# Kernel optimization log

Hardware: AMD Instinct MI355X
Metric: run time of the kernel (lower is better)

The kernel has to match this reference:

```python
import jax, jax.numpy as jnp
import numpy as np

N_EMB = 1024
N_HEADS = 16
HS = N_EMB // N_HEADS  # 64
BASE = 10000.0


def _rope_cache(T):
    # theta uses dim = n_emb (as in the source), sliced to hs//2 frequencies
    i = jnp.arange(HS // 2, dtype=jnp.float32)
    theta = BASE ** (-2.0 * i / N_EMB)            # [hs/2]
    pos = jnp.arange(T, dtype=jnp.float32)        # [T]
    ang = pos[:, None] * theta[None, :]           # [T, hs/2]
    return jnp.cos(ang), jnp.sin(ang)


def _apply_rope(x, cos, sin):
    # x: [B, T, nh, hs]; rotate consecutive pairs along hs
    b, t, nh, hs = x.shape
    xr = x.reshape(b, t, nh, hs // 2, 2)
    c = cos[None, :, None, :]
    s = sin[None, :, None, :]
    r0 = xr[..., 0] * c - xr[..., 1] * s
    r1 = xr[..., 1] * c + xr[..., 0] * s
    return jnp.stack([r0, r1], axis=-1).reshape(b, t, nh, hs)


def setup_inputs() -> dict:
    key = jax.random.key(0)
    k1, k2, k3, k4 = jax.random.split(key, 4)
    B, T = 2, 2048
    w_std = 0.02
    x = jax.random.normal(k1, (B, T, N_EMB), jnp.float32)
    Wq = jax.random.normal(k2, (N_EMB, N_EMB), jnp.float32) * w_std
    Wk = jax.random.normal(k3, (N_EMB, N_EMB), jnp.float32) * w_std
    Wv = jax.random.normal(k4, (N_EMB, N_EMB), jnp.float32) * w_std
    return {"x": x, "Wq": Wq, "Wk": Wk, "Wv": Wv}


def reference(x, Wq, Wk, Wv):
    B, T, C = x.shape
    # nn.Linear(bias=False): y = x @ W.T
    q = (x @ Wq.T).reshape(B, T, N_HEADS, HS)
    k = (x @ Wk.T).reshape(B, T, N_HEADS, HS)
    v = (x @ Wv.T).reshape(B, T, N_HEADS, HS)
    cos, sin = _rope_cache(T)
    q = _apply_rope(q, cos, sin)
    k = _apply_rope(k, cos, sin)
    # scale uses C (n_emb), as in the source (not head_size)
    wei = jnp.einsum('bqhd,bkhd->bhqk', q, k) * (C ** -0.5)  # [B, nh, T, T]
    mask = jnp.tril(jnp.ones((T, T), dtype=bool))
    wei = jnp.where(mask[None, None], wei, -jnp.inf)
    wei = jax.nn.softmax(wei, axis=-1)
    # dropout is identity in eval mode
    out = jnp.einsum('bhqk,bkhd->bqhd', wei, v).reshape(B, T, C)
    return out
```

## Files before the change

kernel.cpp:

```cpp
#include <hip/hip_runtime.h>
#include <stdint.h>

typedef unsigned short u16;
typedef __bf16 bf16x8 __attribute__((ext_vector_type(8)));
typedef unsigned short u16x8 __attribute__((ext_vector_type(8)));
typedef unsigned short u16x4 __attribute__((ext_vector_type(4)));
typedef float f32x4 __attribute__((ext_vector_type(4)));
typedef uint32_t u32v4 __attribute__((ext_vector_type(4)));

#define LOG2E 1.4426950408889634f

typedef const __attribute__((address_space(1))) uint32_t as1_u32;
typedef __attribute__((address_space(3))) uint32_t as3_u32;

__device__ __forceinline__ u16 f2bf(float f) {
  union { float f; uint32_t i; } v; v.f = f;
  uint32_t r = (v.i + 0x7fffu + ((v.i >> 16) & 1u)) >> 16;
  return (u16)r;
}
__device__ __forceinline__ float bf2f(u16 u) {
  union { uint32_t i; float f; } v; v.i = ((uint32_t)u) << 16; return v.f;
}

__device__ __forceinline__ void gld_lds16(const void* g, void* l) {
  as1_u32* gp = (as1_u32*)((uintptr_t)g);
  as3_u32* lp = (as3_u32*)(uint32_t)(uintptr_t)(l);
  __builtin_amdgcn_global_load_lds(gp, lp, 16, 0, 0);
}

__global__ __launch_bounds__(256) void f32_to_bf16(
    const float* __restrict__ x, const float* __restrict__ wq,
    const float* __restrict__ wk, const float* __restrict__ wv,
    u16* __restrict__ xc, u16* __restrict__ wqc,
    u16* __restrict__ wkc, u16* __restrict__ wvc) {
  const int z = blockIdx.y;
  const float* src = z == 0 ? x : (z == 1 ? wq : (z == 2 ? wk : wv));
  u16* dst = z == 0 ? xc : (z == 1 ? wqc : (z == 2 ? wkc : wvc));
  const int n = z == 0 ? (1 << 22) : (1 << 20);

  const int idx = (blockIdx.x * 256 + (int)threadIdx.x) * 8;
  if (idx >= n) return;
  const f32x4 a = *(const f32x4*)&src[idx];
  const f32x4 b = *(const f32x4*)&src[idx + 4];
  u16x8 o;
#pragma unroll
  for (int j = 0; j < 4; j++) { o[j] = f2bf(a[j]); o[j + 4] = f2bf(b[j]); }
  *(u16x8*)&dst[idx] = o;
}

__global__ __launch_bounds__(256) void qkv_gemm(
    const u16* __restrict__ xc, const u16* __restrict__ wqc,
    const u16* __restrict__ wkc, const u16* __restrict__ wvc,
    u16* __restrict__ qo, u16* __restrict__ ko, u16* __restrict__ vt) {
  __shared__ __align__(16) u16 As[128 * 32];
  __shared__ __align__(16) u16 Bs[128 * 32];

  const int tid = threadIdx.x;
  const int lane = tid & 63;
  const int w = tid >> 6;
  const int wm = w >> 1, wn = w & 1;
  const int quad = lane >> 4, m16 = lane & 15;
  const int which = blockIdx.z;

  const u16* __restrict__ Ap;
  const u16* __restrict__ Bp;
  int m0, n0;
  if (which == 2) {
    Ap = wvc; Bp = xc;
    m0 = blockIdx.x * 128;
    n0 = blockIdx.y * 128;
  } else {
    Ap = xc; Bp = which == 0 ? wqc : wkc;
    m0 = blockIdx.y * 128;
    n0 = blockIdx.x * 128;
  }

  const f32x4 z4 = {0.f, 0.f, 0.f, 0.f};
  f32x4 acc[4][4];
#pragma unroll
  for (int i = 0; i < 4; i++)
#pragma unroll
    for (int j = 0; j < 4; j++) acc[i][j] = z4;

  const int rowA = m0 + w * 32 + (lane >> 2);
  const int rowB = n0 + w * 32 + (lane >> 2);
  const int cch = (lane & 3) * 8;

  for (int k0 = 0; k0 < 1024; k0 += 32) {
    __syncthreads();
#pragma unroll
    for (int i = 0; i < 2; i++) {
      gld_lds16(&Ap[(size_t)(rowA + i * 16) * 1024 + k0 + cch],
                &As[(w * 32 + i * 16) * 32]);
      gld_lds16(&Bp[(size_t)(rowB + i * 16) * 1024 + k0 + cch],
                &Bs[(w * 32 + i * 16) * 32]);
    }
    __syncthreads();

    bf16x8 af[4], bfr[4];
#pragma unroll
    for (int t = 0; t < 4; t++) {
      af[t]  = *(const bf16x8*)&As[(wm * 64 + t * 16 + m16) * 32 + quad * 8];
      bfr[t] = *(const bf16x8*)&Bs[(wn * 64 + t * 16 + m16) * 32 + quad * 8];
    }
#pragma unroll
    for (int mt = 0; mt < 4; mt++)
#pragma unroll
      for (int nt = 0; nt < 4; nt++)
        acc[mt][nt] = __builtin_amdgcn_mfma_f32_16x16x32_bf16(
            af[mt], bfr[nt], acc[mt][nt], 0, 0, 0);
  }

  if (which < 2) {
    u16* __restrict__ out = which == 0 ? qo : ko;
#pragma unroll
    for (int mt = 0; mt < 4; mt++) {
      const int row = m0 + wm * 64 + mt * 16 + quad * 4;
#pragma unroll
      for (int nt = 0; nt < 4; nt++) {
        const int n = n0 + wn * 64 + nt * 16 + m16;
        f32x4 a = acc[mt][nt];
#pragma unroll
        for (int r = 0; r < 4; r++)
          out[(size_t)(row + r) * 1024 + n] = f2bf(a[r]);
      }
    }
  } else {
#pragma unroll
    for (int mt = 0; mt < 4; mt++) {
      const int row = m0 + wm * 64 + mt * 16 + quad * 4;
#pragma unroll
      for (int nt = 0; nt < 4; nt++) {
        const int n = n0 + wn * 64 + nt * 16 + m16;
        f32x4 a = acc[mt][nt];
#pragma unroll
        for (int r = 0; r < 4; r++)
          vt[(size_t)(row + r) * 4096 + n] = f2bf(a[r]);
      }
    }
  }
}

__global__ __launch_bounds__(256) void rope_inplace(u16* __restrict__ qb,
                                                    u16* __restrict__ kb) {
  u16* buf = blockIdx.y == 0 ? qb : kb;
  const int p = blockIdx.x * 256 + (int)threadIdx.x;
  const int nidx = p * 2;
  const int row = nidx >> 10;
  const int col = nidx & 1023;
  const int i = (col & 63) >> 1;
  const int t = row & 2047;
  const float theta = exp2f(-(float)i * 0.02595256324130752f);
  const float ang = (float)t * theta;
  float s, c;
  sincosf(ang, &s, &c);
  const float a0 = bf2f(buf[(size_t)row * 1024 + col]);
  const float a1 = bf2f(buf[(size_t)row * 1024 + col + 1]);
  buf[(size_t)row * 1024 + col]     = f2bf(a0 * c - a1 * s);
  buf[(size_t)row * 1024 + col + 1] = f2bf(a1 * c + a0 * s);
}

__global__ __launch_bounds__(256, 4) void flash_attn(
    const u16* __restrict__ qg, const u16* __restrict__ kg,
    const u16* __restrict__ vt, float* __restrict__ out) {
  __shared__ __align__(16) u16 Ks[128 * 72];
  __shared__ __align__(16) u16 Vs[64 * 136];

  const int tid = threadIdx.x, lane = tid & 63, w = tid >> 6;
  const int quad = lane >> 4, m16 = lane & 15;

  const int id  = (int)blockIdx.x;
  const int wid = (id & 7) * 128 + (id >> 3);
  const int uu  = wid & 31;
  const int v   = wid >> 5;
  const int qt  = (v & 1) ? (31 - uu) : uu;
  const int h   = v & 15;
  const int b   = v >> 4;

  const size_t base = (size_t)b * 2048 * 1024 + (size_t)h * 64;
  const size_t vbase = (size_t)(h * 64) * 4096 + (size_t)b * 2048;
  const float SC = 0.03125f * LOG2E;

  const f32x4 z4 = {0.f, 0.f, 0.f, 0.f};
  const int srow = tid >> 2, sc = (tid & 3) * 16;

  union { u16x8 u; bf16x8 f; } ones;
#pragma unroll
  for (int j = 0; j < 8; j++) ones.u[j] = 0x3F80;

  const int q0 = qt * 64;
  const int nr = (qt + 2) >> 1;

  const u16* qsrc = &qg[base + (size_t)(q0 + w * 16 + m16) * 1024 + quad * 8];
  const bf16x8 qf0 = *(const bf16x8*)qsrc;
  const bf16x8 qf1 = *(const bf16x8*)(qsrc + 32);

  u16x8 kr0, kr1, kr2, kr3, vr0, vr1, vr2, vr3;
  {
    const u16* ks = &kg[base + (size_t)srow * 1024 + sc];
    kr0 = *(const u16x8*)ks; kr1 = *(const u16x8*)(ks + 8);
    const u16* ks2 = ks + (size_t)64 * 1024;
    kr2 = *(const u16x8*)ks2; kr3 = *(const u16x8*)(ks2 + 8);
    const u16* vs = &vt[vbase + (size_t)srow * 4096 + sc];
    vr0 = *(const u16x8*)vs; vr1 = *(const u16x8*)(vs + 8);
    vr2 = *(const u16x8*)(vs + 64); vr3 = *(const u16x8*)(vs + 72);
  }

  f32x4 l4 = z4;
  f32x4 O[4];
#pragma unroll
  for (int d = 0; d < 4; d++) O[d] = z4;

  const int qrow0 = q0 + w * 16 + quad * 4;
  const int qcol  = q0 + w * 16 + m16;

  for (int rr = 0; rr < nr; ++rr) {
    const int k0 = rr * 128;
    if (rr) __syncthreads();
    *(u16x8*)&Ks[srow * 72 + sc] = kr0;
    *(u16x8*)&Ks[srow * 72 + sc + 8] = kr1;
    *(u16x8*)&Ks[(64 + srow) * 72 + sc] = kr2;
    *(u16x8*)&Ks[(64 + srow) * 72 + sc + 8] = kr3;
    {
      const u16x4* v0 = (const u16x4*)&vr0;
      const u16x4* v1 = (const u16x4*)&vr1;
      *(u16x4*)&Vs[srow * 136 + sc]      = v0[0];
      *(u16x4*)&Vs[srow * 136 + sc + 4]  = v1[0];
      *(u16x4*)&Vs[srow * 136 + sc + 8]  = v0[1];
      *(u16x4*)&Vs[srow * 136 + sc + 12] = v1[1];
      const u16x4* v2 = (const u16x4*)&vr2;
      const u16x4* v3 = (const u16x4*)&vr3;
      *(u16x4*)&Vs[srow * 136 + 64 + sc]      = v2[0];
      *(u16x4*)&Vs[srow * 136 + 64 + sc + 4]  = v3[0];
      *(u16x4*)&Vs[srow * 136 + 64 + sc + 8]  = v2[1];
      *(u16x4*)&Vs[srow * 136 + 64 + sc + 12] = v3[1];
    }
    __syncthreads();
    if (rr + 1 < nr) {
      const u16* ks = &kg[base + (size_t)(k0 + 128 + srow) * 1024 + sc];
      kr0 = *(const u16x8*)ks; kr1 = *(const u16x8*)(ks + 8);
      const u16* ks2 = ks + (size_t)64 * 1024;
      kr2 = *(const u16x8*)ks2; kr3 = *(const u16x8*)(ks2 + 8);
      const u16* vs = &vt[vbase + (size_t)srow * 4096 + k0 + 128 + sc];
      vr0 = *(const u16x8*)vs; vr1 = *(const u16x8*)(vs + 8);
      vr2 = *(const u16x8*)(vs + 64); vr3 = *(const u16x8*)(vs + 72);
    }

    f32x4 S[8];
#pragma unroll
    for (int nt = 0; nt < 8; nt++) {
      const bf16x8 kf0 = *(const bf16x8*)&Ks[(nt * 16 + m16) * 72 + quad * 8];
      const bf16x8 kf1 =
          *(const bf16x8*)&Ks[(nt * 16 + m16) * 72 + 32 + quad * 8];
      S[nt] = __builtin_amdgcn_mfma_f32_16x16x32_bf16(kf0, qf0, z4, 0, 0, 0);
      S[nt] = __builtin_amdgcn_mfma_f32_16x16x32_bf16(kf1, qf1, S[nt], 0, 0, 0);
    }

    const bool lastr = (rr == nr - 1);
    uint32_t W[16];
#pragma unroll
    for (int nt = 0; nt < 8; nt++) {
      float p[4];
#pragma unroll
      for (int r = 0; r < 4; r++) {
        float e = exp2f(S[nt][r] * SC);
        const int key = k0 + nt * 16 + quad * 4 + r;
        if (lastr && key > qcol) e = 0.f;
        p[r] = e;
      }
      uint32_t w0, w1;
      asm("v_cvt_pk_bf16_f32 %0, %1, %2" : "=v"(w0) : "v"(p[0]), "v"(p[1]));
      asm("v_cvt_pk_bf16_f32 %0, %1, %2" : "=v"(w1) : "v"(p[2]), "v"(p[3]));
      W[2 * nt] = w0; W[2 * nt + 1] = w1;
    }

    union { u32v4 u; bf16x8 f; } P[4];
#pragma unroll
    for (int ks = 0; ks < 4; ks++) {
      uint32_t a0 = W[4 * ks], b0 = W[4 * ks + 2];
      uint32_t a1 = W[4 * ks + 1], b1 = W[4 * ks + 3];
      asm("v_permlane32_swap_b32 %0, %1" : "+v"(a0), "+v"(b0));
      asm("v_permlane32_swap_b32 %0, %1" : "+v"(a1), "+v"(b1));
      P[ks].u = (u32v4){a0, a1, b0, b1};
    }

#pragma unroll
    for (int ks = 0; ks < 4; ks++)
      l4 = __builtin_amdgcn_mfma_f32_16x16x32_bf16(P[ks].f, ones.f, l4,
                                                   0, 0, 0);

#pragma unroll
    for (int dt = 0; dt < 4; dt++) {
#pragma unroll
      for (int ks = 0; ks < 4; ks++) {
        const bf16x8 vf =
            *(const bf16x8*)&Vs[(dt * 16 + m16) * 136 + ks * 32 + quad * 8];
        O[dt] = __builtin_amdgcn_mfma_f32_16x16x32_bf16(P[ks].f, vf, O[dt],
                                                        0, 0, 0);
      }
    }
  }

  float inv[4];
#pragma unroll
  for (int r = 0; r < 4; r++) inv[r] = 1.0f / l4[r];

#pragma unroll
  for (int dt = 0; dt < 4; dt++)
#pragma unroll
    for (int r = 0; r < 4; r++)
      out[base + (size_t)(qrow0 + r) * 1024 + dt * 16 + m16] =
          O[dt][r] * inv[r];
}

extern "C" void kernel_launch(void* const* d_in, const int* in_sizes, int n_in,
                              void* d_out, int out_size, void* d_ws, size_t ws_size,
                              hipStream_t stream) {
  const float* x  = (const float*)d_in[0];
  const float* Wq = (const float*)d_in[1];
  const float* Wk = (const float*)d_in[2];
  const float* Wv = (const float*)d_in[3];
  u16* qb  = (u16*)d_ws;
  u16* kb  = qb  + (size_t)4096 * 1024;
  u16* vtw = kb  + (size_t)4096 * 1024;
  u16* xc  = vtw + (size_t)4096 * 1024;
  u16* wqc = xc  + (size_t)4096 * 1024;
  u16* wkc = wqc + (size_t)1024 * 1024;
  u16* wvc = wkc + (size_t)1024 * 1024;

  f32_to_bf16<<<dim3(2048, 4), 256, 0, stream>>>(x, Wq, Wk, Wv,
                                                 xc, wqc, wkc, wvc);
  qkv_gemm<<<dim3(8, 32, 3), 256, 0, stream>>>(xc, wqc, wkc, wvc,
                                               qb, kb, vtw);
  rope_inplace<<<dim3(8192, 2), 256, 0, stream>>>(qb, kb);
  flash_attn<<<dim3(1024, 1, 1), 256, 0, stream>>>(qb, kb, vtw, (float*)d_out);
}
```

Measured before the change: 165.8 us.

## Widen GEMM K-tile with swizzled LDS, vectorize RoPE, reorder attention blocks

The QKV GEMM now loads a 64-wide K slice per iteration into XOR-swizzled LDS, which halves the barrier count and avoids bank conflicts. The V-transpose output columns are permuted so flash attention can store V into LDS with full 16-byte writes. RoPE processes 8 elements per thread using hardware v_exp/v_sin/v_cos, and softmax uses raw v_exp_f32. Flash attention block scheduling is changed to launch the longest causal q-tiles first. The hardware sin/cos and exp are less accurate, and the permuted V layout has to match how the attention kernel reads it.

```diff
diff --git a/kernel.cpp b/kernel.cpp
--- a/kernel.cpp
+++ b/kernel.cpp
@@ -26,6 +26,12 @@
   as1_u32* gp = (as1_u32*)((uintptr_t)g);
   as3_u32* lp = (as3_u32*)(uint32_t)(uintptr_t)(l);
   __builtin_amdgcn_global_load_lds(gp, lp, 16, 0, 0);
+}
+
+__device__ __forceinline__ float fast_exp2(float x) {
+  float r;
+  asm("v_exp_f32 %0, %1" : "=v"(r) : "v"(x));
+  return r;
 }
 
 __global__ __launch_bounds__(256) void f32_to_bf16(
@@ -52,8 +58,8 @@
     const u16* __restrict__ xc, const u16* __restrict__ wqc,
     const u16* __restrict__ wkc, const u16* __restrict__ wvc,
     u16* __restrict__ qo, u16* __restrict__ ko, u16* __restrict__ vt) {
-  __shared__ __align__(16) u16 As[128 * 32];
-  __shared__ __align__(16) u16 Bs[128 * 32];
+  __shared__ __align__(16) u16 As[128 * 64];
+  __shared__ __align__(16) u16 Bs[128 * 64];
 
   const int tid = threadIdx.x;
   const int lane = tid & 63;
@@ -82,33 +88,42 @@
 #pragma unroll
     for (int j = 0; j < 4; j++) acc[i][j] = z4;
 
-  const int rowA = m0 + w * 32 + (lane >> 2);
-  const int rowB = n0 + w * 32 + (lane >> 2);
-  const int cch = (lane & 3) * 8;
-
-  for (int k0 = 0; k0 < 1024; k0 += 32) {
+  const int lrow = lane >> 3;
+  const int scol = ((lane & 7) ^ (lrow & 7)) * 8;
+  const int srowA = m0 + w * 32 + lrow;
+  const int srowB = n0 + w * 32 + lrow;
+  const int rsw = m16 & 7;
+
+  for (int k0 = 0; k0 < 1024; k0 += 64) {
     __syncthreads();
 #pragma unroll
-    for (int i = 0; i < 2; i++) {
-      gld_lds16(&Ap[(size_t)(rowA + i * 16) * 1024 + k0 + cch],
-                &As[(w * 32 + i * 16) * 32]);
-      gld_lds16(&Bp[(size_t)(rowB + i * 16) * 1024 + k0 + cch],
-                &Bs[(w * 32 + i * 16) * 32]);
+    for (int j = 0; j < 4; j++) {
+      gld_lds16(&Ap[(size_t)(srowA + j * 8) * 1024 + k0 + scol],
+                &As[(w * 32 + j * 8) * 64]);
+      gld_lds16(&Bp[(size_t)(srowB + j * 8) * 1024 + k0 + scol],
+                &Bs[(w * 32 + j * 8) * 64]);
     }
     __syncthreads();
 
-    bf16x8 af[4], bfr[4];
-#pragma unroll
-    for (int t = 0; t < 4; t++) {
-      af[t]  = *(const bf16x8*)&As[(wm * 64 + t * 16 + m16) * 32 + quad * 8];
-      bfr[t] = *(const bf16x8*)&Bs[(wn * 64 + t * 16 + m16) * 32 + quad * 8];
-    }
-#pragma unroll
-    for (int mt = 0; mt < 4; mt++)
-#pragma unroll
-      for (int nt = 0; nt < 4; nt++)
-        acc[mt][nt] = __builtin_amdgcn_mfma_f32_16x16x32_bf16(
-            af[mt], bfr[nt], acc[mt][nt], 0, 0, 0);
+#pragma unroll
+    for (int kk = 0; kk < 2; kk++) {
+      bf16x8 af[4], bfr[4];
+      const int csw = ((kk * 4) ^ rsw) * 8;
+#pragma unroll
+      for (int t = 0; t < 4; t++) {
+        af[t] = *(const bf16x8*)
+            &As[(wm * 64 + t * 16 + m16) * 64 + (((kk * 4 + quad) ^ rsw) * 8)];
+        bfr[t] = *(const bf16x8*)
+            &Bs[(wn * 64 + t * 16 + m16) * 64 + (((kk * 4 + quad) ^ rsw) * 8)];
+      }
+      (void)csw;
+#pragma unroll
+      for (int mt = 0; mt < 4; mt++)
+#pragma unroll
+        for (int nt = 0; nt < 4; nt++)
+          acc[mt][nt] = __builtin_amdgcn_mfma_f32_16x16x32_bf16(
+              af[mt], bfr[nt], acc[mt][nt], 0, 0, 0);
+    }
   }
 
   if (which < 2) {
@@ -126,12 +141,13 @@
       }
     }
   } else {
+    const int m16p = (m16 & 3) | ((m16 & 4) << 1) | ((m16 & 8) >> 1);
 #pragma unroll
     for (int mt = 0; mt < 4; mt++) {
       const int row = m0 + wm * 64 + mt * 16 + quad * 4;
 #pragma unroll
       for (int nt = 0; nt < 4; nt++) {
-        const int n = n0 + wn * 64 + nt * 16 + m16;
+        const int n = n0 + wn * 64 + nt * 16 + m16p;
         f32x4 a = acc[mt][nt];
 #pragma unroll
         for (int r = 0; r < 4; r++)
@@ -145,19 +161,28 @@
                                                     u16* __restrict__ kb) {
   u16* buf = blockIdx.y == 0 ? qb : kb;
   const int p = blockIdx.x * 256 + (int)threadIdx.x;
-  const int nidx = p * 2;
-  const int row = nidx >> 10;
-  const int col = nidx & 1023;
-  const int i = (col & 63) >> 1;
+  const int e0 = p * 8;
+  const int row = e0 >> 10;
+  const int col0 = e0 & 1023;
   const int t = row & 2047;
-  const float theta = exp2f(-(float)i * 0.02595256324130752f);
-  const float ang = (float)t * theta;
-  float s, c;
-  sincosf(ang, &s, &c);
-  const float a0 = bf2f(buf[(size_t)row * 1024 + col]);
-  const float a1 = bf2f(buf[(size_t)row * 1024 + col + 1]);
-  buf[(size_t)row * 1024 + col]     = f2bf(a0 * c - a1 * s);
-  buf[(size_t)row * 1024 + col + 1] = f2bf(a1 * c + a0 * s);
+  const float tf = (float)t;
+
+  u16x8 d = *(const u16x8*)&buf[(size_t)row * 1024 + col0];
+  u16x8 o;
+#pragma unroll
+  for (int j = 0; j < 4; j++) {
+    const int i = ((col0 & 63) >> 1) + j;
+    const float th = fast_exp2(-(float)i * 0.02595256324130752f);
+    const float rev = tf * th * 0.15915494309189535f;
+    float fr, s, c;
+    asm("v_fract_f32 %0, %1" : "=v"(fr) : "v"(rev));
+    asm("v_sin_f32 %0, %1" : "=v"(s) : "v"(fr));
+    asm("v_cos_f32 %0, %1" : "=v"(c) : "v"(fr));
+    const float a0 = bf2f(d[2 * j]), a1 = bf2f(d[2 * j + 1]);
+    o[2 * j]     = f2bf(a0 * c - a1 * s);
+    o[2 * j + 1] = f2bf(a1 * c + a0 * s);
+  }
+  *(u16x8*)&buf[(size_t)row * 1024 + col0] = o;
 }
 
 __global__ __launch_bounds__(256, 4) void flash_attn(
@@ -169,24 +194,24 @@
   const int tid = threadIdx.x, lane = tid & 63, w = tid >> 6;
   const int quad = lane >> 4, m16 = lane & 15;
 
-  const int id  = (int)blockIdx.x;
-  const int wid = (id & 7) * 128 + (id >> 3);
-  const int uu  = wid & 31;
-  const int v   = wid >> 5;
-  const int qt  = (v & 1) ? (31 - uu) : uu;
-  const int h   = v & 15;
-  const int b   = v >> 4;
-
-  const size_t base = (size_t)b * 2048 * 1024 + (size_t)h * 64;
+  const int id   = (int)blockIdx.x;
+  const int X    = id & 7;
+  const int rem  = id >> 3;
+  const int qt   = 31 - (rem >> 2);
+  const int vloc = rem & 3;
+  const int v    = X * 4 + vloc;
+  const int h    = v & 15;
+  const int b    = v >> 4;
+
+  const size_t base  = (size_t)b * 2048 * 1024 + (size_t)h * 64;
   const size_t vbase = (size_t)(h * 64) * 4096 + (size_t)b * 2048;
   const float SC = 0.03125f * LOG2E;
-
   const f32x4 z4 = {0.f, 0.f, 0.f, 0.f};
   const int srow = tid >> 2, sc = (tid & 3) * 16;
 
   union { u16x8 u; bf16x8 f; } ones;
 #pragma unroll
-  for (int j = 0; j < 8; j++) ones.u[j] = 0x3F80;
+  for (int k = 0; k < 8; k++) ones.u[k] = 0x3F80;
 
   const int q0 = qt * 64;
   const int nr = (qt + 2) >> 1;
@@ -221,20 +246,10 @@
     *(u16x8*)&Ks[srow * 72 + sc + 8] = kr1;
     *(u16x8*)&Ks[(64 + srow) * 72 + sc] = kr2;
     *(u16x8*)&Ks[(64 + srow) * 72 + sc + 8] = kr3;
-    {
-      const u16x4* v0 = (const u16x4*)&vr0;
-      const u16x4* v1 = (const u16x4*)&vr1;
-      *(u16x4*)&Vs[srow * 136 + sc]      = v0[0];
-      *(u16x4*)&Vs[srow * 136 + sc + 4]  = v1[0];
-      *(u16x4*)&Vs[srow * 136 + sc + 8]  = v0[1];
-      *(u16x4*)&Vs[srow * 136 + sc + 12] = v1[1];
-      const u16x4* v2 = (const u16x4*)&vr2;
-      const u16x4* v3 = (const u16x4*)&vr3;
-      *(u16x4*)&Vs[srow * 136 + 64 + sc]      = v2[0];
-      *(u16x4*)&Vs[srow * 136 + 64 + sc + 4]  = v3[0];
-      *(u16x4*)&Vs[srow * 136 + 64 + sc + 8]  = v2[1];
-      *(u16x4*)&Vs[srow * 136 + 64 + sc + 12] = v3[1];
-    }
+    *(u16x8*)&Vs[srow * 136 + sc] = vr0;
+    *(u16x8*)&Vs[srow * 136 + sc + 8] = vr1;
+    *(u16x8*)&Vs[srow * 136 + 64 + sc] = vr2;
+    *(u16x8*)&Vs[srow * 136 + 64 + sc + 8] = vr3;
     __syncthreads();
     if (rr + 1 < nr) {
       const u16* ks = &kg[base + (size_t)(k0 + 128 + srow) * 1024 + sc];
@@ -263,7 +278,7 @@
       float p[4];
 #pragma unroll
       for (int r = 0; r < 4; r++) {
-        float e = exp2f(S[nt][r] * SC);
+        float e = fast_exp2(S[nt][r] * SC);
         const int key = k0 + nt * 16 + quad * 4 + r;
         if (lastr && key > qcol) e = 0.f;
         p[r] = e;
@@ -332,6 +347,6 @@
                                                  xc, wqc, wkc, wvc);
   qkv_gemm<<<dim3(8, 32, 3), 256, 0, stream>>>(xc, wqc, wkc, wvc,
                                                qb, kb, vtw);
-  rope_inplace<<<dim3(8192, 2), 256, 0, stream>>>(qb, kb);
+  rope_inplace<<<dim3(2048, 2), 256, 0, stream>>>(qb, kb);
   flash_attn<<<dim3(1024, 1, 1), 256, 0, stream>>>(qb, kb, vtw, (float*)d_out);
 }
```

Result: faster. 153.5 us (-7.4%).
